# Kernel optimization log

Hardware: AMD Instinct MI355X
Metric: run time of the kernel (lower is better)

The kernel has to match this reference:

```python
import jax, jax.numpy as jnp
import numpy as np

B, L, D = 32, 2048, 768
H = 512
EPS = 1e-5  # batch_norm eps (PyG MLP default norm)


def setup_inputs() -> dict:
    key = jax.random.key(0)
    ks = jax.random.split(key, 8)
    hidden = jax.random.normal(ks[0], (B, L, D), dtype=jnp.float32)
    attention_mask = jax.random.randint(ks[1], (B, L), 0, 2, dtype=jnp.int32)
    W1 = jax.random.normal(ks[2], (D, H), dtype=jnp.float32) * 0.02
    b1 = jnp.zeros((H,), dtype=jnp.float32)
    gamma = jnp.ones((H,), dtype=jnp.float32)
    beta = jnp.zeros((H,), dtype=jnp.float32)
    W2 = jax.random.normal(ks[3], (H, H), dtype=jnp.float32) * 0.02
    b2 = jnp.zeros((H,), dtype=jnp.float32)
    return {"hidden": hidden, "attention_mask": attention_mask,
            "W1": W1, "b1": b1, "gamma": gamma, "beta": beta,
            "W2": W2, "b2": b2}


def reference(hidden, attention_mask, W1, b1, gamma, beta, W2, b2):
    # Valid-token mask; pads are excluded from the batched graph's node set.
    m = attention_mask.astype(hidden.dtype)[..., None]  # (B, L, 1)
    n_valid = jnp.maximum(jnp.sum(m), 1.0)

    # MLP layer 1: Linear -> BatchNorm (stats over all valid nodes across the
    # whole batched graph, mirroring PyG MLP training-mode batch_norm) -> ReLU
    h = jnp.einsum('bld,dh->blh', hidden, W1) + b1  # (B, L, H)
    mean = jnp.sum(h * m, axis=(0, 1)) / n_valid
    var = jnp.sum(jnp.square(h - mean) * m, axis=(0, 1)) / n_valid
    h = (h - mean) * jax.lax.rsqrt(var + EPS) * gamma + beta
    h = jax.nn.relu(h)

    # MLP layer 2 (plain_last: no norm/act)
    out = jnp.einsum('blh,hk->blk', h, W2) + b2  # (B, L, H)

    # scores == ones -> segment softmax over each sequence's valid tokens is
    # uniform 1/n_b; scatter_add over batch ids == masked mean pool.
    counts = jnp.maximum(jnp.sum(m, axis=1), 1.0)  # (B, 1)
    pooled = jnp.sum(out * m, axis=1) / counts  # (B, H)
    return pooled
```

## Files before the change

### kernel.cpp

```cpp
#include <hip/hip_runtime.h>
#include <hip/hip_bf16.h>

#define Bn 32
#define Ln 2048
#define Dn 768
#define Hn 512
#define Mn (Bn*Ln)
#define EPSC 1e-5f

#define OFF_S1   0
#define OFF_S2   512
#define OFF_CNT  2048
#define OFF_PH   2304
#define OFF_W1T_BYTES  131072
#define OFF_H_BYTES    1048576

#define BM 128
#define BN2 256
#define BK 64
#define LDK 72

typedef __attribute__((ext_vector_type(8))) short bf16x8;
typedef __attribute__((ext_vector_type(4))) float f32x4;

static __device__ __forceinline__ unsigned short f2bf(float x) {
  __hip_bfloat16 h = __float2bfloat16(x);
  return *reinterpret_cast<unsigned short*>(&h);
}
static __device__ __forceinline__ float bf2f(unsigned short u) {
  return __uint_as_float(((unsigned int)u) << 16);
}

__global__ __launch_bounds__(256) void pre_kernel(const int* __restrict__ mask,
                                                  float* __restrict__ ws) {
  int blk = blockIdx.x, t = threadIdx.x;
  if (blk < Bn) {
    __shared__ int red[256];
    int s = 0;
#pragma unroll
    for (int i = 0; i < 8; i++) s += mask[blk * Ln + i * 256 + t];
    red[t] = s;
    __syncthreads();
    for (int off = 128; off > 0; off >>= 1) {
      if (t < off) red[t] += red[t + off];
      __syncthreads();
    }
    if (t == 0) ws[OFF_CNT + blk] = (float)red[0];
  } else {
#pragma unroll
    for (int i = 0; i < 4; i++) ws[OFF_S1 + i * 256 + t] = 0.f;
#pragma unroll
    for (int i = 0; i < 64; i++) ws[OFF_PH + i * 256 + t] = 0.f;
  }
}

__global__ __launch_bounds__(256) void transpose_w1(
    const float* __restrict__ W1, unsigned short* __restrict__ W1t) {
  __shared__ float tile[32][33];
  int kx = blockIdx.x * 32;
  int nx = blockIdx.y * 32;
  int tx = threadIdx.x & 31, ty = threadIdx.x >> 5;
#pragma unroll
  for (int i = 0; i < 32; i += 8)
    tile[ty + i][tx] = W1[(size_t)(kx + ty + i) * Hn + nx + tx];
  __syncthreads();
#pragma unroll
  for (int i = 0; i < 32; i += 8)
    W1t[(size_t)(nx + ty + i) * Dn + kx + tx] = f2bf(tile[tx][ty + i]);
}

__global__ __launch_bounds__(512, 4) void gemm1_mfma(
    const float* __restrict__ A, const unsigned short* __restrict__ W1t,
    const float* __restrict__ b1, const int* __restrict__ mask,
    unsigned short* __restrict__ Hout,
    float* __restrict__ gsum, float* __restrict__ gsq)
{
  __shared__ unsigned short As[BM * LDK];
  __shared__ unsigned short Bs[BN2 * LDK];
  __shared__ float csum[BN2];
  __shared__ float csq[BN2];

  const int t = threadIdx.x;
  const int bx = blockIdx.x;
  const int by = blockIdx.y;
  const int bm0 = by * BM;
  const int bn0 = bx * BN2;

  const int w = t >> 6;
  const int lane = t & 63;
  const int wm0 = (w >> 2) * 64;
  const int wn0 = (w & 3) * 64;
  const int l15 = lane & 15;
  const int quad = lane >> 4;

  const int am = t >> 2;
  const int ak = (t & 3) * 16;
  const int bn = t >> 1;
  const int bk = (t & 1) * 32;

  const float* Ap = A + (size_t)(bm0 + am) * Dn + ak;
  const unsigned short* Bp = W1t + (size_t)(bn0 + bn) * Dn + bk;

  f32x4 acc[4][4];
#pragma unroll
  for (int i = 0; i < 4; i++)
#pragma unroll
    for (int j = 0; j < 4; j++) acc[i][j] = (f32x4){0.f, 0.f, 0.f, 0.f};

  for (int k0 = 0; k0 < Dn; k0 += BK) {
    float4 a0 = *(const float4*)(Ap + k0);
    float4 a1 = *(const float4*)(Ap + k0 + 4);
    float4 a2 = *(const float4*)(Ap + k0 + 8);
    float4 a3 = *(const float4*)(Ap + k0 + 12);
    uint4 bv0 = *(const uint4*)(Bp + k0);
    uint4 bv1 = *(const uint4*)(Bp + k0 + 8);
    uint4 bv2 = *(const uint4*)(Bp + k0 + 16);
    uint4 bv3 = *(const uint4*)(Bp + k0 + 24);
    __syncthreads();
    uint4 p0, p1;
    p0.x = (unsigned int)f2bf(a0.x) | ((unsigned int)f2bf(a0.y) << 16);
    p0.y = (unsigned int)f2bf(a0.z) | ((unsigned int)f2bf(a0.w) << 16);
    p0.z = (unsigned int)f2bf(a1.x) | ((unsigned int)f2bf(a1.y) << 16);
    p0.w = (unsigned int)f2bf(a1.z) | ((unsigned int)f2bf(a1.w) << 16);
    p1.x = (unsigned int)f2bf(a2.x) | ((unsigned int)f2bf(a2.y) << 16);
    p1.y = (unsigned int)f2bf(a2.z) | ((unsigned int)f2bf(a2.w) << 16);
    p1.z = (unsigned int)f2bf(a3.x) | ((unsigned int)f2bf(a3.y) << 16);
    p1.w = (unsigned int)f2bf(a3.z) | ((unsigned int)f2bf(a3.w) << 16);
    *(uint4*)&As[am * LDK + ak] = p0;
    *(uint4*)&As[am * LDK + ak + 8] = p1;
    *(uint4*)&Bs[bn * LDK + bk] = bv0;
    *(uint4*)&Bs[bn * LDK + bk + 8] = bv1;
    *(uint4*)&Bs[bn * LDK + bk + 16] = bv2;
    *(uint4*)&Bs[bn * LDK + bk + 24] = bv3;
    __syncthreads();
#pragma unroll
    for (int s = 0; s < 2; s++) {
      bf16x8 af[4], bf[4];
#pragma unroll
      for (int mt = 0; mt < 4; mt++)
        af[mt] = *(const bf16x8*)&As[(wm0 + mt * 16 + l15) * LDK + s * 32 + quad * 8];
#pragma unroll
      for (int nt = 0; nt < 4; nt++)
        bf[nt] = *(const bf16x8*)&Bs[(wn0 + nt * 16 + l15) * LDK + s * 32 + quad * 8];
#pragma unroll
      for (int mt = 0; mt < 4; mt++)
#pragma unroll
        for (int nt = 0; nt < 4; nt++)
          acc[mt][nt] = __builtin_amdgcn_mfma_f32_16x16x32_bf16(
              af[mt], bf[nt], acc[mt][nt], 0, 0, 0);
    }
  }

  if (t < BN2) { csum[t] = 0.f; csq[t] = 0.f; }
  __syncthreads();

  float mk[4][4];
#pragma unroll
  for (int mt = 0; mt < 4; mt++) {
    int4 mv = *(const int4*)(mask + bm0 + wm0 + mt * 16 + quad * 4);
    mk[mt][0] = (float)mv.x; mk[mt][1] = (float)mv.y;
    mk[mt][2] = (float)mv.z; mk[mt][3] = (float)mv.w;
  }

  const size_t cbase = ((size_t)(by * 2 + bx)) * 32768 + (size_t)w * 4096;
#pragma unroll
  for (int nt = 0; nt < 4; nt++) {
    const int nl = wn0 + nt * 16 + l15;
    const float bias = b1[bn0 + nl];
    float ps = 0.f, pq = 0.f;
#pragma unroll
    for (int mt = 0; mt < 4; mt++) {
      ushort4 st;
      float v0 = acc[mt][nt][0] + bias;
      float v1 = acc[mt][nt][1] + bias;
      float v2 = acc[mt][nt][2] + bias;
      float v3 = acc[mt][nt][3] + bias;
      ps += v0 * mk[mt][0] + v1 * mk[mt][1] + v2 * mk[mt][2] + v3 * mk[mt][3];
      pq += v0 * v0 * mk[mt][0] + v1 * v1 * mk[mt][1] +
            v2 * v2 * mk[mt][2] + v3 * v3 * mk[mt][3];
      st.x = f2bf(v0); st.y = f2bf(v1); st.z = f2bf(v2); st.w = f2bf(v3);
      *(ushort4*)&Hout[cbase + (size_t)(mt * 4 + nt) * 256 + lane * 4] = st;
    }
    atomicAdd(&csum[nl], ps);
    atomicAdd(&csq[nl], pq);
  }

  __syncthreads();
  if (t < BN2) {
    atomicAdd(&gsum[bn0 + t], csum[t]);
    atomicAdd(&gsq[bn0 + t], csq[t]);
  }
}

__global__ __launch_bounds__(256) void bnpool_kernel(
    const unsigned short* __restrict__ Hbuf, const int* __restrict__ mask,
    const float* __restrict__ ws, const float* __restrict__ gamma,
    const float* __restrict__ beta, float* __restrict__ PH)
{
  __shared__ float mkf[BM];
  __shared__ float redc[32];
  const int t = threadIdx.x;
  const int chunk = blockIdx.x;
  const int by = chunk >> 1, bx = chunk & 1;
  const int b = chunk >> 5;
  if (t < 32) redc[t] = ws[OFF_CNT + t];
  if (t < BM) mkf[t] = (float)mask[by * BM + t];
  __syncthreads();

  float nv = 0.f;
#pragma unroll
  for (int i = 0; i < 32; i++) nv += redc[i];
  nv = fmaxf(nv, 1.f);
  const float inv = 1.f / nv;
  const int c = bx * BN2 + t;
  const float m = ws[OFF_S1 + c] * inv;
  const float var = ws[OFF_S2 + c] * inv - m * m;
  const float istd = rsqrtf(fmaxf(var, 0.f) + EPSC);
  const float scv = istd * gamma[c];
  const float shv = beta[c] - m * scv;

  const int w3 = t >> 6, nt = (t >> 4) & 3, l15 = t & 15;
  float acc = 0.f;
#pragma unroll
  for (int h = 0; h < 2; h++) {
    const int w = w3 + h * 4;
    const int wm0 = h * 64;
    const unsigned short* base =
        Hbuf + (size_t)chunk * 32768 + (size_t)w * 4096 + nt * 256 + l15 * 4;
#pragma unroll
    for (int mt = 0; mt < 4; mt++)
#pragma unroll
      for (int q = 0; q < 4; q++) {
        ushort4 hv = *(const ushort4*)(base + mt * 1024 + q * 64);
        const float* mv = &mkf[wm0 + mt * 16 + q * 4];
        acc += fmaxf(fmaf(bf2f(hv.x), scv, shv), 0.f) * mv[0]
             + fmaxf(fmaf(bf2f(hv.y), scv, shv), 0.f) * mv[1]
             + fmaxf(fmaf(bf2f(hv.z), scv, shv), 0.f) * mv[2]
             + fmaxf(fmaf(bf2f(hv.w), scv, shv), 0.f) * mv[3];
      }
  }
  atomicAdd(&PH[b * Hn + c], acc);
}

__global__ __launch_bounds__(128) void final_kernel(
    const float* __restrict__ pooledh, const float* __restrict__ cnt,
    const float* __restrict__ W2, const float* __restrict__ b2,
    float* __restrict__ out)
{
  __shared__ float pr[Hn];
  int b = blockIdx.x >> 2;
  int cc = blockIdx.x & 3;
  int t = threadIdx.x;
  float nb = cnt[b];
  float inv = 1.f / fmaxf(nb, 1.f);
#pragma unroll
  for (int i = 0; i < 4; i++)
    pr[t + i * 128] = pooledh[b * Hn + t + i * 128] * inv;
  __syncthreads();
  int c = cc * 128 + t;
  float a0 = 0.f, a1 = 0.f, a2 = 0.f, a3 = 0.f;
  for (int i = 0; i < Hn; i += 4) {
    a0 = fmaf(pr[i],     W2[(size_t)i * Hn + c],       a0);
    a1 = fmaf(pr[i + 1], W2[(size_t)(i + 1) * Hn + c], a1);
    a2 = fmaf(pr[i + 2], W2[(size_t)(i + 2) * Hn + c], a2);
    a3 = fmaf(pr[i + 3], W2[(size_t)(i + 3) * Hn + c], a3);
  }
  out[b * Hn + c] = (a0 + a1) + (a2 + a3) + b2[c] * (nb * inv);
}

extern "C" void kernel_launch(void* const* d_in, const int* in_sizes, int n_in,
                              void* d_out, int out_size, void* d_ws, size_t ws_size,
                              hipStream_t stream) {
  const float* hidden = (const float*)d_in[0];
  const int*   mask   = (const int*)d_in[1];
  const float* W1     = (const float*)d_in[2];
  const float* b1     = (const float*)d_in[3];
  const float* gamma  = (const float*)d_in[4];
  const float* beta   = (const float*)d_in[5];
  const float* W2     = (const float*)d_in[6];
  const float* b2     = (const float*)d_in[7];
  float* out = (float*)d_out;
  float* ws  = (float*)d_ws;
  unsigned short* W1t  = (unsigned short*)((char*)d_ws + OFF_W1T_BYTES);
  unsigned short* Hbuf = (unsigned short*)((char*)d_ws + OFF_H_BYTES);

  pre_kernel<<<Bn + 1, 256, 0, stream>>>(mask, ws);
  transpose_w1<<<dim3(Dn / 32, Hn / 32), 256, 0, stream>>>(W1, W1t);
  gemm1_mfma<<<dim3(Hn / BN2, Mn / BM), 512, 0, stream>>>(
      hidden, W1t, b1, mask, Hbuf, ws + OFF_S1, ws + OFF_S2);
  bnpool_kernel<<<(Mn / BM) * (Hn / BN2), 256, 0, stream>>>(
      Hbuf, mask, ws, gamma, beta, ws + OFF_PH);
  final_kernel<<<Bn * 4, 128, 0, stream>>>(ws + OFF_PH, ws + OFF_CNT, W2, b2, out);
}
```

Measured before the change: 390.7 us.

## Retile GEMM1 to 64x256 blocks with XOR-swizzled LDS and shuffle-reduced stats

Shrinks the GEMM1 block tile from 128 to 64 rows and uses 256 threads. Each wave now computes a 32x128 sub-tile, which gives more B-fragment reuse per A fragment. Padded shared-memory rows are replaced by an XOR swizzle to avoid bank conflicts. BN statistics are reduced with wave shuffles and written with direct global atomics instead of shared-memory atomics. The bnpool kernel is updated to match the new H buffer layout. The cost is twice as many blocks, more global atomic traffic, and more A reloads per W1 tile.

```diff
diff --git a/kernel.cpp b/kernel.cpp
--- a/kernel.cpp
+++ b/kernel.cpp
@@ -15,10 +15,9 @@
 #define OFF_W1T_BYTES  131072
 #define OFF_H_BYTES    1048576
 
-#define BM 128
+#define BM 64
 #define BN2 256
 #define BK 64
-#define LDK 72
 
 typedef __attribute__((ext_vector_type(8))) short bf16x8;
 typedef __attribute__((ext_vector_type(4))) float f32x4;
@@ -26,6 +25,9 @@
 static __device__ __forceinline__ unsigned short f2bf(float x) {
   __hip_bfloat16 h = __float2bfloat16(x);
   return *reinterpret_cast<unsigned short*>(&h);
+}
+static __device__ __forceinline__ unsigned int pk2(float lo, float hi) {
+  return (unsigned int)f2bf(lo) | ((unsigned int)f2bf(hi) << 16);
 }
 static __device__ __forceinline__ float bf2f(unsigned short u) {
   return __uint_as_float(((unsigned int)u) << 16);
@@ -69,16 +71,14 @@
     W1t[(size_t)(nx + ty + i) * Dn + kx + tx] = f2bf(tile[tx][ty + i]);
 }
 
-__global__ __launch_bounds__(512, 4) void gemm1_mfma(
+__global__ __launch_bounds__(256) void gemm1_mfma(
     const float* __restrict__ A, const unsigned short* __restrict__ W1t,
     const float* __restrict__ b1, const int* __restrict__ mask,
     unsigned short* __restrict__ Hout,
     float* __restrict__ gsum, float* __restrict__ gsq)
 {
-  __shared__ unsigned short As[BM * LDK];
-  __shared__ unsigned short Bs[BN2 * LDK];
-  __shared__ float csum[BN2];
-  __shared__ float csq[BN2];
+  __shared__ unsigned short As[BM * BK];
+  __shared__ unsigned short Bs[BN2 * BK];
 
   const int t = threadIdx.x;
   const int bx = blockIdx.x;
@@ -88,88 +88,83 @@
 
   const int w = t >> 6;
   const int lane = t & 63;
-  const int wm0 = (w >> 2) * 64;
-  const int wn0 = (w & 3) * 64;
+  const int wm0 = (w >> 1) * 32;
+  const int wn0 = (w & 1) * 128;
   const int l15 = lane & 15;
   const int quad = lane >> 4;
-
-  const int am = t >> 2;
-  const int ak = (t & 3) * 16;
-  const int bn = t >> 1;
-  const int bk = (t & 1) * 32;
-
-  const float* Ap = A + (size_t)(bm0 + am) * Dn + ak;
-  const unsigned short* Bp = W1t + (size_t)(bn0 + bn) * Dn + bk;
-
-  f32x4 acc[4][4];
-#pragma unroll
-  for (int i = 0; i < 4; i++)
-#pragma unroll
-    for (int j = 0; j < 4; j++) acc[i][j] = (f32x4){0.f, 0.f, 0.f, 0.f};
+  const int lsw = l15 & 7;
+
+  const int arow = t >> 2;
+  const int akc = (t & 3) * 2;
+  const float* Ap = A + (size_t)(bm0 + arow) * Dn + akc * 8;
+  unsigned short* As0 = &As[arow * 64 + ((akc) ^ (arow & 7)) * 8];
+  unsigned short* As1 = &As[arow * 64 + ((akc + 1) ^ (arow & 7)) * 8];
+
+  const unsigned short* Bp = W1t + (size_t)(bn0 + t) * Dn;
+  unsigned short* Bsrow = &Bs[t * 64];
+  const int bsw = t & 7;
+
+  f32x4 acc[2][8];
+#pragma unroll
+  for (int i = 0; i < 2; i++)
+#pragma unroll
+    for (int j = 0; j < 8; j++) acc[i][j] = (f32x4){0.f, 0.f, 0.f, 0.f};
 
   for (int k0 = 0; k0 < Dn; k0 += BK) {
     float4 a0 = *(const float4*)(Ap + k0);
     float4 a1 = *(const float4*)(Ap + k0 + 4);
     float4 a2 = *(const float4*)(Ap + k0 + 8);
     float4 a3 = *(const float4*)(Ap + k0 + 12);
-    uint4 bv0 = *(const uint4*)(Bp + k0);
-    uint4 bv1 = *(const uint4*)(Bp + k0 + 8);
-    uint4 bv2 = *(const uint4*)(Bp + k0 + 16);
-    uint4 bv3 = *(const uint4*)(Bp + k0 + 24);
+    uint4 bv[8];
+#pragma unroll
+    for (int j = 0; j < 8; j++) bv[j] = *(const uint4*)(Bp + k0 + j * 8);
     __syncthreads();
     uint4 p0, p1;
-    p0.x = (unsigned int)f2bf(a0.x) | ((unsigned int)f2bf(a0.y) << 16);
-    p0.y = (unsigned int)f2bf(a0.z) | ((unsigned int)f2bf(a0.w) << 16);
-    p0.z = (unsigned int)f2bf(a1.x) | ((unsigned int)f2bf(a1.y) << 16);
-    p0.w = (unsigned int)f2bf(a1.z) | ((unsigned int)f2bf(a1.w) << 16);
-    p1.x = (unsigned int)f2bf(a2.x) | ((unsigned int)f2bf(a2.y) << 16);
-    p1.y = (unsigned int)f2bf(a2.z) | ((unsigned int)f2bf(a2.w) << 16);
-    p1.z = (unsigned int)f2bf(a3.x) | ((unsigned int)f2bf(a3.y) << 16);
-    p1.w = (unsigned int)f2bf(a3.z) | ((unsigned int)f2bf(a3.w) << 16);
-    *(uint4*)&As[am * LDK + ak] = p0;
-    *(uint4*)&As[am * LDK + ak + 8] = p1;
-    *(uint4*)&Bs[bn * LDK + bk] = bv0;
-    *(uint4*)&Bs[bn * LDK + bk + 8] = bv1;
-    *(uint4*)&Bs[bn * LDK + bk + 16] = bv2;
-    *(uint4*)&Bs[bn * LDK + bk + 24] = bv3;
+    p0.x = pk2(a0.x, a0.y); p0.y = pk2(a0.z, a0.w);
+    p0.z = pk2(a1.x, a1.y); p0.w = pk2(a1.z, a1.w);
+    p1.x = pk2(a2.x, a2.y); p1.y = pk2(a2.z, a2.w);
+    p1.z = pk2(a3.x, a3.y); p1.w = pk2(a3.z, a3.w);
+    *(uint4*)As0 = p0;
+    *(uint4*)As1 = p1;
+#pragma unroll
+    for (int j = 0; j < 8; j++)
+      *(uint4*)&Bsrow[(j ^ bsw) * 8] = bv[j];
     __syncthreads();
 #pragma unroll
     for (int s = 0; s < 2; s++) {
-      bf16x8 af[4], bf[4];
-#pragma unroll
-      for (int mt = 0; mt < 4; mt++)
-        af[mt] = *(const bf16x8*)&As[(wm0 + mt * 16 + l15) * LDK + s * 32 + quad * 8];
-#pragma unroll
-      for (int nt = 0; nt < 4; nt++)
-        bf[nt] = *(const bf16x8*)&Bs[(wn0 + nt * 16 + l15) * LDK + s * 32 + quad * 8];
-#pragma unroll
-      for (int mt = 0; mt < 4; mt++)
-#pragma unroll
-        for (int nt = 0; nt < 4; nt++)
+      const int csw = ((s * 4 + quad) ^ lsw) * 8;
+      bf16x8 af[2], bf[8];
+#pragma unroll
+      for (int mt = 0; mt < 2; mt++)
+        af[mt] = *(const bf16x8*)&As[(wm0 + mt * 16 + l15) * 64 + csw];
+#pragma unroll
+      for (int nt = 0; nt < 8; nt++)
+        bf[nt] = *(const bf16x8*)&Bs[(wn0 + nt * 16 + l15) * 64 + csw];
+#pragma unroll
+      for (int mt = 0; mt < 2; mt++)
+#pragma unroll
+        for (int nt = 0; nt < 8; nt++)
           acc[mt][nt] = __builtin_amdgcn_mfma_f32_16x16x32_bf16(
               af[mt], bf[nt], acc[mt][nt], 0, 0, 0);
     }
   }
 
-  if (t < BN2) { csum[t] = 0.f; csq[t] = 0.f; }
-  __syncthreads();
-
-  float mk[4][4];
-#pragma unroll
-  for (int mt = 0; mt < 4; mt++) {
+  float mk[2][4];
+#pragma unroll
+  for (int mt = 0; mt < 2; mt++) {
     int4 mv = *(const int4*)(mask + bm0 + wm0 + mt * 16 + quad * 4);
     mk[mt][0] = (float)mv.x; mk[mt][1] = (float)mv.y;
     mk[mt][2] = (float)mv.z; mk[mt][3] = (float)mv.w;
   }
 
-  const size_t cbase = ((size_t)(by * 2 + bx)) * 32768 + (size_t)w * 4096;
-#pragma unroll
-  for (int nt = 0; nt < 4; nt++) {
+  const size_t cbase = ((size_t)(by * 2 + bx)) * 16384 + (size_t)w * 4096;
+#pragma unroll
+  for (int nt = 0; nt < 8; nt++) {
     const int nl = wn0 + nt * 16 + l15;
     const float bias = b1[bn0 + nl];
     float ps = 0.f, pq = 0.f;
 #pragma unroll
-    for (int mt = 0; mt < 4; mt++) {
+    for (int mt = 0; mt < 2; mt++) {
       ushort4 st;
       float v0 = acc[mt][nt][0] + bias;
       float v1 = acc[mt][nt][1] + bias;
@@ -179,16 +174,16 @@
       pq += v0 * v0 * mk[mt][0] + v1 * v1 * mk[mt][1] +
             v2 * v2 * mk[mt][2] + v3 * v3 * mk[mt][3];
       st.x = f2bf(v0); st.y = f2bf(v1); st.z = f2bf(v2); st.w = f2bf(v3);
-      *(ushort4*)&Hout[cbase + (size_t)(mt * 4 + nt) * 256 + lane * 4] = st;
-    }
-    atomicAdd(&csum[nl], ps);
-    atomicAdd(&csq[nl], pq);
-  }
-
-  __syncthreads();
-  if (t < BN2) {
-    atomicAdd(&gsum[bn0 + t], csum[t]);
-    atomicAdd(&gsq[bn0 + t], csq[t]);
+      *(ushort4*)&Hout[cbase + (size_t)(mt * 8 + nt) * 256 + lane * 4] = st;
+    }
+    ps += __shfl_xor(ps, 16);
+    ps += __shfl_xor(ps, 32);
+    pq += __shfl_xor(pq, 16);
+    pq += __shfl_xor(pq, 32);
+    if (quad == 0) {
+      atomicAdd(&gsum[bn0 + nl], ps);
+      atomicAdd(&gsq[bn0 + nl], pq);
+    }
   }
 }
 
@@ -201,8 +196,8 @@
   __shared__ float redc[32];
   const int t = threadIdx.x;
   const int chunk = blockIdx.x;
-  const int by = chunk >> 1, bx = chunk & 1;
-  const int b = chunk >> 5;
+  const int by = chunk >> 1, bxh = chunk & 1;
+  const int b = by >> 5;
   if (t < 32) redc[t] = ws[OFF_CNT + t];
   if (t < BM) mkf[t] = (float)mask[by * BM + t];
   __syncthreads();
@@ -212,27 +207,26 @@
   for (int i = 0; i < 32; i++) nv += redc[i];
   nv = fmaxf(nv, 1.f);
   const float inv = 1.f / nv;
-  const int c = bx * BN2 + t;
+  const int c = bxh * BN2 + t;
   const float m = ws[OFF_S1 + c] * inv;
   const float var = ws[OFF_S2 + c] * inv - m * m;
   const float istd = rsqrtf(fmaxf(var, 0.f) + EPSC);
   const float scv = istd * gamma[c];
   const float shv = beta[c] - m * scv;
 
-  const int w3 = t >> 6, nt = (t >> 4) & 3, l15 = t & 15;
+  const int wlo = t >> 7, nt = (t >> 4) & 7, l15 = t & 15;
   float acc = 0.f;
 #pragma unroll
   for (int h = 0; h < 2; h++) {
-    const int w = w3 + h * 4;
-    const int wm0 = h * 64;
+    const int w = h * 2 + wlo;
     const unsigned short* base =
-        Hbuf + (size_t)chunk * 32768 + (size_t)w * 4096 + nt * 256 + l15 * 4;
-#pragma unroll
-    for (int mt = 0; mt < 4; mt++)
+        Hbuf + (size_t)chunk * 16384 + (size_t)w * 4096 + nt * 256 + l15 * 4;
+#pragma unroll
+    for (int mt = 0; mt < 2; mt++)
 #pragma unroll
       for (int q = 0; q < 4; q++) {
-        ushort4 hv = *(const ushort4*)(base + mt * 1024 + q * 64);
-        const float* mv = &mkf[wm0 + mt * 16 + q * 4];
+        ushort4 hv = *(const ushort4*)(base + mt * 2048 + q * 64);
+        const float* mv = &mkf[h * 32 + mt * 16 + q * 4];
         acc += fmaxf(fmaf(bf2f(hv.x), scv, shv), 0.f) * mv[0]
              + fmaxf(fmaf(bf2f(hv.y), scv, shv), 0.f) * mv[1]
              + fmaxf(fmaf(bf2f(hv.z), scv, shv), 0.f) * mv[2]
@@ -286,7 +280,7 @@
 
   pre_kernel<<<Bn + 1, 256, 0, stream>>>(mask, ws);
   transpose_w1<<<dim3(Dn / 32, Hn / 32), 256, 0, stream>>>(W1, W1t);
-  gemm1_mfma<<<dim3(Hn / BN2, Mn / BM), 512, 0, stream>>>(
+  gemm1_mfma<<<dim3(Hn / BN2, Mn / BM), 256, 0, stream>>>(
       hidden, W1t, b1, mask, Hbuf, ws + OFF_S1, ws + OFF_S2);
   bnpool_kernel<<<(Mn / BM) * (Hn / BN2), 256, 0, stream>>>(
       Hbuf, mask, ws, gamma, beta, ws + OFF_PH);
```

Result: slower. 627.3 us (+60.5%).
